# Kernel optimization log

Measured on AMD Instinct MI355X. Metric: run time of the kernel, lower is better.

The kernel has to match this reference:

```python
import jax, jax.numpy as jnp
import numpy as np

SHAPELET_SIZE = 64
NUM_SHAPELETS = 128
IN_CHANNELS = 8


def setup_inputs() -> dict:
    key = jax.random.key(0)
    k1, k2 = jax.random.split(key)
    x = jax.random.normal(k1, (64, IN_CHANNELS, 2048), dtype=jnp.float32)
    shapelets = jax.random.normal(k2, (IN_CHANNELS, NUM_SHAPELETS, SHAPELET_SIZE), dtype=jnp.float32)
    return {"x": x, "shapelets": shapelets}


def _znorm(s):
    # Z-normalize along the time-step axis (dim 2), matching Znormalize_dim(shapelets, 2)
    mu = jnp.mean(s, axis=2, keepdims=True)
    sd = jnp.std(s, axis=2, keepdims=True)
    return (s - mu) / sd


def reference(x, shapelets):
    # x: (N, C, L); shapelets: (C, K, S)
    S = shapelets.shape[-1]
    N, C, L = x.shape
    W = L - S + 1
    # unfold(2, S, 1): sliding windows -> (N, C, W, S)
    idx = jnp.arange(W)[:, None] + jnp.arange(S)[None, :]  # (W, S)
    xw = x[:, :, idx]  # (N, C, W, S)
    sh = _znorm(shapelets)  # (C, K, S)
    # Euclidean cdist via ||a||^2 + ||b||^2 - 2 a.b (avoids (N,C,W,K,S) blowup)
    sq_x = jnp.sum(xw * xw, axis=-1)          # (N, C, W)
    sq_s = jnp.sum(sh * sh, axis=-1)          # (C, K)
    cross = jnp.einsum('ncws,cks->ncwk', xw, sh)  # (N, C, W, K)
    d2 = sq_x[..., None] + sq_s[None, :, None, :] - 2.0 * cross
    d = jnp.sqrt(jnp.maximum(d2, 1e-12))      # (N, C, W, K)
    # sum over channels, then global min over windows -> (N, 1, K)
    dsum = jnp.sum(d, axis=1)                 # (N, W, K)
    out = jnp.min(dsum, axis=1)[:, None, :]   # (N, 1, K)
    return out
```

## Files before the change

kernel.cpp:

```cpp
#include <hip/hip_runtime.h>
#include <hip/hip_bf16.h>
#include <math.h>

#define C 8
#define K 128
#define S 64
#define L 2048
#define NB 64
#define W (L - S + 1)
#define TW 128
#define NTW 16
#define NKB 2
#define XCS 208
#define XFS 200

typedef __attribute__((ext_vector_type(8))) short bf16x8;
typedef __attribute__((ext_vector_type(4))) float f32x4;

__device__ __forceinline__ unsigned short f2bf(float f) {
  unsigned int u = __float_as_uint(f);
  u += 0x7FFFu + ((u >> 16) & 1u);
  return (unsigned short)(u >> 16);
}

__device__ __forceinline__ unsigned int pkbf(float a, float b) {
  __hip_bfloat162 h = __float22bfloat162_rn(make_float2(a, b));
  return *reinterpret_cast<unsigned int*>(&h);
}

__device__ __forceinline__ void gll16(const void* g, void* l) {
  __builtin_amdgcn_global_load_lds((const __attribute__((address_space(1))) void*)g,
                                   (__attribute__((address_space(3))) void*)l, 16, 0, 0);
}

__global__ __launch_bounds__(256) void prep_kernel(const float* __restrict__ sh,
                                                   unsigned short* __restrict__ shzB,
                                                   float* __restrict__ out) {
  int tid = blockIdx.x * 256 + threadIdx.x;
  if (tid < NB * K) out[tid] = __int_as_float(0x7F800000);
  int gid = blockIdx.x * 4 + (threadIdx.x >> 6);
  int lane = threadIdx.x & 63;
  float v = sh[(size_t)gid * S + lane];
  float s1 = v, s2 = v * v;
#pragma unroll
  for (int off = 32; off > 0; off >>= 1) {
    s1 += __shfl_down(s1, off);
    s2 += __shfl_down(s2, off);
  }
  s1 = __shfl(s1, 0);
  s2 = __shfl(s2, 0);
  float mu = s1 * (1.0f / S);
  float sd = sqrtf(fmaxf(s2 * (1.0f / S) - mu * mu, 0.0f));
  float z = (v - mu) / sd;
  int c = gid >> 7, k = gid & (K - 1), s = lane;
  int idx = (k >> 6) * 32768 + c * 4096 + ((((k >> 4) & 3) * 2) + (s >> 5)) * 512 +
            ((((s >> 3) & 3) * 16 + (k & 15)) * 8) + (s & 7);
  shzB[idx] = f2bf(-2.0f * z);
}

__global__ __launch_bounds__(512, 4) void main_kernel(const float* __restrict__ x,
                                                      const unsigned short* __restrict__ shzB,
                                                      int* __restrict__ out) {
  __shared__ __align__(16) unsigned short bbuf[4096];
  __shared__ __align__(16) unsigned short xcop[C][8][XCS];
  __shared__ __align__(16) float sqx[C][TW];

  const int t = threadIdx.x;
  const int lane = t & 63;
  const int wave = t >> 6;
  const int wgrp = wave & 1;
  const int kgrp = wave >> 1;
  const int col = lane & 15;
  const int quad = lane >> 4;
  const int n = blockIdx.z;
  const int kblk = blockIdx.y;
  const int w0 = blockIdx.x * TW;
  const float* xn = x + (size_t)n * C * L;
  const unsigned short* bsrc = shzB + kblk * 32768;

  float* xf = (float*)bbuf;
  {
    const int c = wave;
    const int e = lane * 4;
    float4 v; v.x = v.y = v.z = v.w = 0.0f;
    if (lane < 48) {
      int g = w0 + e;
      if (g + 3 < L) {
        v = *(const float4*)(xn + c * L + g);
      } else {
        v.x = (g + 0 < L) ? xn[c * L + g + 0] : 0.0f;
        v.y = (g + 1 < L) ? xn[c * L + g + 1] : 0.0f;
        v.z = (g + 2 < L) ? xn[c * L + g + 2] : 0.0f;
        v.w = (g + 3 < L) ? xn[c * L + g + 3] : 0.0f;
      }
    }
    if (lane < 50) *(float4*)&xf[c * XFS + e] = v;
  }
  __syncthreads();

  {
    const int cb = wave;
    const int rb = lane >> 3;
    const int c8 = lane & 7;
    const float* xr = xf + cb * XFS;
#pragma unroll
    for (int j = 0; j < 12; ++j) {
      int i = (c8 + j * 8) * 2;
      *(unsigned int*)&xcop[cb][rb][i] = pkbf(xr[i + rb], xr[i + rb + 1]);
    }
  }
  {
    const int c = wave, wl = lane * 2;
    const float* xr = xf + c * XFS;
    float p0 = 0.f, p1 = 0.f, p2 = 0.f, p3 = 0.f;
#pragma unroll
    for (int si = 0; si < S; si += 4) {
      float v0 = xr[wl + si], v1 = xr[wl + si + 1], v2 = xr[wl + si + 2], v3 = xr[wl + si + 3];
      p0 = fmaf(v0, v0, p0); p1 = fmaf(v1, v1, p1);
      p2 = fmaf(v2, v2, p2); p3 = fmaf(v3, v3, p3);
    }
    float s0 = 64.0f + (p0 + p1) + (p2 + p3);
    sqx[c][wl] = s0;
    float a = xr[wl + S], b = xr[wl];
    sqx[c][wl + 1] = s0 + a * a - b * b;
  }
  __syncthreads();

  gll16(bsrc + t * 8, &bbuf[wave * 512]);

  const f32x4 z4 = {0.0f, 0.0f, 0.0f, 0.0f};
  f32x4 dsum[4];
#pragma unroll
  for (int a = 0; a < 4; ++a) dsum[a] = z4;

  const int r8 = col & 7;
  const int abase = wgrp * 64 + (col - r8) + quad * 8;

  for (int c = 0; c < C; ++c) {
    __syncthreads();
    bf16x8 b0 = *(const bf16x8*)(&bbuf[(kgrp * 2 + 0) * 512 + lane * 8]);
    bf16x8 b1 = *(const bf16x8*)(&bbuf[(kgrp * 2 + 1) * 512 + lane * 8]);
    __syncthreads();

    if (c + 1 < C)
      gll16(bsrc + (c + 1) * 4096 + t * 8, &bbuf[wave * 512]);

    f32x4 acc[4];
#pragma unroll
    for (int wt = 0; wt < 4; ++wt)
      acc[wt] = *(const f32x4*)&sqx[c][wgrp * 64 + wt * 16 + quad * 4];
    const unsigned short* xc = &xcop[c][r8][0];
#pragma unroll
    for (int wt = 0; wt < 4; ++wt) {
      bf16x8 a0 = *(const bf16x8*)(xc + abase + wt * 16);
      acc[wt] = __builtin_amdgcn_mfma_f32_16x16x32_bf16(a0, b0, acc[wt], 0, 0, 0);
    }
#pragma unroll
    for (int wt = 0; wt < 4; ++wt) {
      bf16x8 a1 = *(const bf16x8*)(xc + abase + wt * 16 + 32);
      acc[wt] = __builtin_amdgcn_mfma_f32_16x16x32_bf16(a1, b1, acc[wt], 0, 0, 0);
    }
#pragma unroll
    for (int wt = 0; wt < 4; ++wt)
#pragma unroll
      for (int i = 0; i < 4; ++i)
        dsum[wt][i] += __builtin_amdgcn_sqrtf(fmaxf(acc[wt][i], 0.0f));
  }

  const float INF = __int_as_float(0x7F800000);
  int wbase = w0 + wgrp * 64;
  float mv = INF;
#pragma unroll
  for (int wt = 0; wt < 4; ++wt)
#pragma unroll
    for (int i = 0; i < 4; ++i) {
      int w = wbase + wt * 16 + quad * 4 + i;
      mv = (w < W) ? fminf(mv, dsum[wt][i]) : mv;
    }
  mv = fminf(mv, __shfl_xor(mv, 16));
  mv = fminf(mv, __shfl_xor(mv, 32));
  if (quad == 0)
    atomicMin(&out[n * K + kblk * 64 + kgrp * 16 + col], __float_as_int(mv));
}

extern "C" void kernel_launch(void* const* d_in, const int* in_sizes, int n_in,
                              void* d_out, int out_size, void* d_ws, size_t ws_size,
                              hipStream_t stream) {
  const float* x = (const float*)d_in[0];
  const float* sh = (const float*)d_in[1];
  float* out = (float*)d_out;
  unsigned short* shzB = (unsigned short*)d_ws;

  prep_kernel<<<256, 256, 0, stream>>>(sh, shzB, out);
  main_kernel<<<dim3(NTW, NKB, NB), 512, 0, stream>>>(x, shzB, (int*)out);
}
```

Baseline: 91.78 us.

## Cover all shapelets per block with 4 k-tiles per wave and double-buffered B

Removes the k-block grid dimension so each 256-thread block handles all 128 shapelets for one window tile. Each wave now computes four 16-wide k tiles, which reuses the A fragments from LDS across four MFMAs, and the per-channel shapelet tiles are double-buffered in LDS so one sync per channel is enough. This halves redundant x loading and packing across blocks, at the cost of more accumulator registers, lower occupancy, and half as many blocks.

```diff
diff --git a/kernel.cpp b/kernel.cpp
--- a/kernel.cpp
+++ b/kernel.cpp
@@ -10,7 +10,6 @@
 #define W (L - S + 1)
 #define TW 128
 #define NTW 16
-#define NKB 2
 #define XCS 208
 #define XFS 200
 
@@ -53,15 +52,15 @@
   float sd = sqrtf(fmaxf(s2 * (1.0f / S) - mu * mu, 0.0f));
   float z = (v - mu) / sd;
   int c = gid >> 7, k = gid & (K - 1), s = lane;
-  int idx = (k >> 6) * 32768 + c * 4096 + ((((k >> 4) & 3) * 2) + (s >> 5)) * 512 +
+  int idx = c * 8192 + (k >> 6) * 4096 + ((((k >> 4) & 3) * 2) + (s >> 5)) * 512 +
             ((((s >> 3) & 3) * 16 + (k & 15)) * 8) + (s & 7);
   shzB[idx] = f2bf(-2.0f * z);
 }
 
-__global__ __launch_bounds__(512, 4) void main_kernel(const float* __restrict__ x,
+__global__ __launch_bounds__(256, 2) void main_kernel(const float* __restrict__ x,
                                                       const unsigned short* __restrict__ shzB,
                                                       int* __restrict__ out) {
-  __shared__ __align__(16) unsigned short bbuf[4096];
+  __shared__ __align__(16) unsigned short bbuf[2][8192];
   __shared__ __align__(16) unsigned short xcop[C][8][XCS];
   __shared__ __align__(16) float sqx[C][TW];
 
@@ -72,15 +71,15 @@
   const int kgrp = wave >> 1;
   const int col = lane & 15;
   const int quad = lane >> 4;
-  const int n = blockIdx.z;
-  const int kblk = blockIdx.y;
+  const int n = blockIdx.y;
   const int w0 = blockIdx.x * TW;
   const float* xn = x + (size_t)n * C * L;
-  const unsigned short* bsrc = shzB + kblk * 32768;
+  const unsigned short* bsrc = shzB;
 
   float* xf = (float*)bbuf;
-  {
-    const int c = wave;
+#pragma unroll
+  for (int cc = 0; cc < 2; ++cc) {
+    const int c = wave * 2 + cc;
     const int e = lane * 4;
     float4 v; v.x = v.y = v.z = v.w = 0.0f;
     if (lane < 48) {
@@ -98,8 +97,9 @@
   }
   __syncthreads();
 
-  {
-    const int cb = wave;
+#pragma unroll
+  for (int cc = 0; cc < 2; ++cc) {
+    const int cb = wave * 2 + cc;
     const int rb = lane >> 3;
     const int c8 = lane & 7;
     const float* xr = xf + cb * XFS;
@@ -109,8 +109,9 @@
       *(unsigned int*)&xcop[cb][rb][i] = pkbf(xr[i + rb], xr[i + rb + 1]);
     }
   }
-  {
-    const int c = wave, wl = lane * 2;
+#pragma unroll
+  for (int cc = 0; cc < 2; ++cc) {
+    const int c = wave * 2 + cc, wl = lane * 2;
     const float* xr = xf + c * XFS;
     float p0 = 0.f, p1 = 0.f, p2 = 0.f, p3 = 0.f;
 #pragma unroll
@@ -126,61 +127,81 @@
   }
   __syncthreads();
 
-  gll16(bsrc + t * 8, &bbuf[wave * 512]);
+#pragma unroll
+  for (int i = 0; i < 4; ++i)
+    gll16(bsrc + i * 2048 + t * 8, &bbuf[0][i * 2048 + wave * 512]);
 
   const f32x4 z4 = {0.0f, 0.0f, 0.0f, 0.0f};
-  f32x4 dsum[4];
-#pragma unroll
-  for (int a = 0; a < 4; ++a) dsum[a] = z4;
+  f32x4 dsum[4][4];
+#pragma unroll
+  for (int kt = 0; kt < 4; ++kt)
+#pragma unroll
+    for (int wt = 0; wt < 4; ++wt) dsum[kt][wt] = z4;
 
   const int r8 = col & 7;
   const int abase = wgrp * 64 + (col - r8) + quad * 8;
 
   for (int c = 0; c < C; ++c) {
     __syncthreads();
-    bf16x8 b0 = *(const bf16x8*)(&bbuf[(kgrp * 2 + 0) * 512 + lane * 8]);
-    bf16x8 b1 = *(const bf16x8*)(&bbuf[(kgrp * 2 + 1) * 512 + lane * 8]);
-    __syncthreads();
-
-    if (c + 1 < C)
-      gll16(bsrc + (c + 1) * 4096 + t * 8, &bbuf[wave * 512]);
-
-    f32x4 acc[4];
+
+    if (c + 1 < C) {
+#pragma unroll
+      for (int i = 0; i < 4; ++i)
+        gll16(bsrc + (c + 1) * 8192 + i * 2048 + t * 8,
+              &bbuf[(c + 1) & 1][i * 2048 + wave * 512]);
+    }
+
+    const unsigned short* bb = &bbuf[c & 1][kgrp * 4096];
+    bf16x8 b00 = *(const bf16x8*)(bb + 0 * 512 + lane * 8);
+    bf16x8 b01 = *(const bf16x8*)(bb + 1 * 512 + lane * 8);
+    bf16x8 b10 = *(const bf16x8*)(bb + 2 * 512 + lane * 8);
+    bf16x8 b11 = *(const bf16x8*)(bb + 3 * 512 + lane * 8);
+    bf16x8 b20 = *(const bf16x8*)(bb + 4 * 512 + lane * 8);
+    bf16x8 b21 = *(const bf16x8*)(bb + 5 * 512 + lane * 8);
+    bf16x8 b30 = *(const bf16x8*)(bb + 6 * 512 + lane * 8);
+    bf16x8 b31 = *(const bf16x8*)(bb + 7 * 512 + lane * 8);
+
+    const unsigned short* xc = &xcop[c][r8][0];
+#pragma unroll
+    for (int wt = 0; wt < 4; ++wt) {
+      f32x4 ai = *(const f32x4*)&sqx[c][wgrp * 64 + wt * 16 + quad * 4];
+      bf16x8 x0 = *(const bf16x8*)(xc + abase + wt * 16);
+      bf16x8 x1 = *(const bf16x8*)(xc + abase + wt * 16 + 32);
+      f32x4 a0 = __builtin_amdgcn_mfma_f32_16x16x32_bf16(x0, b00, ai, 0, 0, 0);
+      f32x4 a1 = __builtin_amdgcn_mfma_f32_16x16x32_bf16(x0, b10, ai, 0, 0, 0);
+      f32x4 a2 = __builtin_amdgcn_mfma_f32_16x16x32_bf16(x0, b20, ai, 0, 0, 0);
+      f32x4 a3 = __builtin_amdgcn_mfma_f32_16x16x32_bf16(x0, b30, ai, 0, 0, 0);
+      a0 = __builtin_amdgcn_mfma_f32_16x16x32_bf16(x1, b01, a0, 0, 0, 0);
+      a1 = __builtin_amdgcn_mfma_f32_16x16x32_bf16(x1, b11, a1, 0, 0, 0);
+      a2 = __builtin_amdgcn_mfma_f32_16x16x32_bf16(x1, b21, a2, 0, 0, 0);
+      a3 = __builtin_amdgcn_mfma_f32_16x16x32_bf16(x1, b31, a3, 0, 0, 0);
+#pragma unroll
+      for (int i = 0; i < 4; ++i) {
+        dsum[0][wt][i] += __builtin_amdgcn_sqrtf(fmaxf(a0[i], 0.0f));
+        dsum[1][wt][i] += __builtin_amdgcn_sqrtf(fmaxf(a1[i], 0.0f));
+        dsum[2][wt][i] += __builtin_amdgcn_sqrtf(fmaxf(a2[i], 0.0f));
+        dsum[3][wt][i] += __builtin_amdgcn_sqrtf(fmaxf(a3[i], 0.0f));
+      }
+    }
+  }
+
+  const float INF = __int_as_float(0x7F800000);
+  const int wbase = w0 + wgrp * 64;
+#pragma unroll
+  for (int kt = 0; kt < 4; ++kt) {
+    float mv = INF;
 #pragma unroll
     for (int wt = 0; wt < 4; ++wt)
-      acc[wt] = *(const f32x4*)&sqx[c][wgrp * 64 + wt * 16 + quad * 4];
-    const unsigned short* xc = &xcop[c][r8][0];
-#pragma unroll
-    for (int wt = 0; wt < 4; ++wt) {
-      bf16x8 a0 = *(const bf16x8*)(xc + abase + wt * 16);
-      acc[wt] = __builtin_amdgcn_mfma_f32_16x16x32_bf16(a0, b0, acc[wt], 0, 0, 0);
-    }
-#pragma unroll
-    for (int wt = 0; wt < 4; ++wt) {
-      bf16x8 a1 = *(const bf16x8*)(xc + abase + wt * 16 + 32);
-      acc[wt] = __builtin_amdgcn_mfma_f32_16x16x32_bf16(a1, b1, acc[wt], 0, 0, 0);
-    }
-#pragma unroll
-    for (int wt = 0; wt < 4; ++wt)
-#pragma unroll
-      for (int i = 0; i < 4; ++i)
-        dsum[wt][i] += __builtin_amdgcn_sqrtf(fmaxf(acc[wt][i], 0.0f));
-  }
-
-  const float INF = __int_as_float(0x7F800000);
-  int wbase = w0 + wgrp * 64;
-  float mv = INF;
-#pragma unroll
-  for (int wt = 0; wt < 4; ++wt)
-#pragma unroll
-    for (int i = 0; i < 4; ++i) {
-      int w = wbase + wt * 16 + quad * 4 + i;
-      mv = (w < W) ? fminf(mv, dsum[wt][i]) : mv;
-    }
-  mv = fminf(mv, __shfl_xor(mv, 16));
-  mv = fminf(mv, __shfl_xor(mv, 32));
-  if (quad == 0)
-    atomicMin(&out[n * K + kblk * 64 + kgrp * 16 + col], __float_as_int(mv));
+#pragma unroll
+      for (int i = 0; i < 4; ++i) {
+        int w = wbase + wt * 16 + quad * 4 + i;
+        mv = (w < W) ? fminf(mv, dsum[kt][wt][i]) : mv;
+      }
+    mv = fminf(mv, __shfl_xor(mv, 16));
+    mv = fminf(mv, __shfl_xor(mv, 32));
+    if (quad == 0)
+      atomicMin(&out[n * K + kgrp * 64 + kt * 16 + col], __float_as_int(mv));
+  }
 }
 
 extern "C" void kernel_launch(void* const* d_in, const int* in_sizes, int n_in,
@@ -192,5 +213,5 @@
   unsigned short* shzB = (unsigned short*)d_ws;
 
   prep_kernel<<<256, 256, 0, stream>>>(sh, shzB, out);
-  main_kernel<<<dim3(NTW, NKB, NB), 512, 0, stream>>>(x, shzB, (int*)out);
-}
+  main_kernel<<<dim3(NTW, NB), 256, 0, stream>>>(x, shzB, (int*)out);
+}
```

Result: no change. 92.28 us (+0.6%).

## Split waves into MFMA producers and sqrt consumers via double-buffered LDS slab

Applied to the files above, without the earlier changes.

Each block now covers all 128 shapelets instead of half. Four waves compute the MFMA distances into a double-buffered LDS slab while the other four waves, at raised priority, apply sqrt and accumulate across channels. B fragments are loaded directly from global memory into registers instead of through LDS, and each block starts at a rotated channel so blocks spread their reads. This aims to overlap the transcendental work with the matrix work and halve the redundant x staging, but it raises LDS use and drops occupancy to one block of 512 threads per CU.

```diff
diff --git a/kernel.cpp b/kernel.cpp
--- a/kernel.cpp
+++ b/kernel.cpp
@@ -10,9 +10,9 @@
 #define W (L - S + 1)
 #define TW 128
 #define NTW 16
-#define NKB 2
 #define XCS 208
 #define XFS 200
+#define SW 72
 
 typedef __attribute__((ext_vector_type(8))) short bf16x8;
 typedef __attribute__((ext_vector_type(4))) float f32x4;
@@ -26,11 +26,6 @@
 __device__ __forceinline__ unsigned int pkbf(float a, float b) {
   __hip_bfloat162 h = __float22bfloat162_rn(make_float2(a, b));
   return *reinterpret_cast<unsigned int*>(&h);
-}
-
-__device__ __forceinline__ void gll16(const void* g, void* l) {
-  __builtin_amdgcn_global_load_lds((const __attribute__((address_space(1))) void*)g,
-                                   (__attribute__((address_space(3))) void*)l, 16, 0, 0);
 }
 
 __global__ __launch_bounds__(256) void prep_kernel(const float* __restrict__ sh,
@@ -53,32 +48,69 @@
   float sd = sqrtf(fmaxf(s2 * (1.0f / S) - mu * mu, 0.0f));
   float z = (v - mu) / sd;
   int c = gid >> 7, k = gid & (K - 1), s = lane;
-  int idx = (k >> 6) * 32768 + c * 4096 + ((((k >> 4) & 3) * 2) + (s >> 5)) * 512 +
+  int idx = c * 8192 + (k >> 6) * 4096 + ((((k >> 4) & 3) * 2) + (s >> 5)) * 512 +
             ((((s >> 3) & 3) * 16 + (k & 15)) * 8) + (s & 7);
   shzB[idx] = f2bf(-2.0f * z);
 }
 
-__global__ __launch_bounds__(512, 4) void main_kernel(const float* __restrict__ x,
+#define PRODUCE(H, SLOT)                                                        \
+  {                                                                             \
+    const unsigned short* xc = &xcop[c][r8][0];                                 \
+    const int wb = (H) * 64 + pw2 * 32;                                         \
+    _Pragma("unroll")                                                           \
+    for (int wt = 0; wt < 2; ++wt) {                                            \
+      f32x4 ai = *(const f32x4*)&sqx[c][wb + wt * 16 + quad * 4];               \
+      bf16x8 x0 = *(const bf16x8*)(xc + alane + wb + wt * 16);                  \
+      bf16x8 x1 = *(const bf16x8*)(xc + alane + wb + wt * 16 + 32);             \
+      _Pragma("unroll")                                                         \
+      for (int kt = 0; kt < 4; ++kt) {                                          \
+        f32x4 acc =                                                             \
+            __builtin_amdgcn_mfma_f32_16x16x32_bf16(x0, Bc[2 * kt], ai, 0, 0, 0);\
+        acc = __builtin_amdgcn_mfma_f32_16x16x32_bf16(x1, Bc[2 * kt + 1], acc,  \
+                                                      0, 0, 0);                 \
+        *(f32x4*)&slab[SLOT][pk * 64 + kt * 16 + col]                           \
+                           [pw2 * 32 + wt * 16 + quad * 4] = acc;               \
+      }                                                                         \
+    }                                                                           \
+  }
+
+#define CONSUME(SLOT, DS)                                                       \
+  {                                                                             \
+    f32x4 r[4][2];                                                              \
+    _Pragma("unroll")                                                           \
+    for (int wt = 0; wt < 4; ++wt)                                              \
+      _Pragma("unroll")                                                         \
+      for (int kl = 0; kl < 2; ++kl)                                            \
+        r[wt][kl] = *(const f32x4*)&slab[SLOT][q * 32 + kl * 16 + col]          \
+                                             [wt * 16 + quad * 4];              \
+    _Pragma("unroll")                                                           \
+    for (int wt = 0; wt < 4; ++wt)                                              \
+      _Pragma("unroll")                                                         \
+      for (int kl = 0; kl < 2; ++kl)                                            \
+        _Pragma("unroll")                                                       \
+        for (int i = 0; i < 4; ++i)                                             \
+          DS[wt][kl][i] +=                                                      \
+              __builtin_amdgcn_sqrtf(__builtin_fabsf(r[wt][kl][i]));            \
+  }
+
+__global__ __launch_bounds__(512, 1) void main_kernel(const float* __restrict__ x,
                                                       const unsigned short* __restrict__ shzB,
                                                       int* __restrict__ out) {
-  __shared__ __align__(16) unsigned short bbuf[4096];
+  __shared__ __align__(16) float slab[2][K][SW];
   __shared__ __align__(16) unsigned short xcop[C][8][XCS];
   __shared__ __align__(16) float sqx[C][TW];
 
   const int t = threadIdx.x;
   const int lane = t & 63;
   const int wave = t >> 6;
-  const int wgrp = wave & 1;
-  const int kgrp = wave >> 1;
   const int col = lane & 15;
   const int quad = lane >> 4;
-  const int n = blockIdx.z;
-  const int kblk = blockIdx.y;
+  const int n = blockIdx.y;
   const int w0 = blockIdx.x * TW;
   const float* xn = x + (size_t)n * C * L;
-  const unsigned short* bsrc = shzB + kblk * 32768;
-
-  float* xf = (float*)bbuf;
+  const int cbase = (blockIdx.x + 3 * blockIdx.y) & 7;
+
+  float* xfp = &slab[0][0][0];
   {
     const int c = wave;
     const int e = lane * 4;
@@ -94,7 +126,7 @@
         v.w = (g + 3 < L) ? xn[c * L + g + 3] : 0.0f;
       }
     }
-    if (lane < 50) *(float4*)&xf[c * XFS + e] = v;
+    if (lane < 50) *(float4*)&xfp[c * XFS + e] = v;
   }
   __syncthreads();
 
@@ -102,7 +134,7 @@
     const int cb = wave;
     const int rb = lane >> 3;
     const int c8 = lane & 7;
-    const float* xr = xf + cb * XFS;
+    const float* xr = xfp + cb * XFS;
 #pragma unroll
     for (int j = 0; j < 12; ++j) {
       int i = (c8 + j * 8) * 2;
@@ -111,7 +143,7 @@
   }
   {
     const int c = wave, wl = lane * 2;
-    const float* xr = xf + c * XFS;
+    const float* xr = xfp + c * XFS;
     float p0 = 0.f, p1 = 0.f, p2 = 0.f, p3 = 0.f;
 #pragma unroll
     for (int si = 0; si < S; si += 4) {
@@ -124,63 +156,71 @@
     float a = xr[wl + S], b = xr[wl];
     sqx[c][wl + 1] = s0 + a * a - b * b;
   }
+
+  const int r8 = col & 7;
+  const int alane = (col - r8) + quad * 8;
+
+  const int pk = wave >> 1;
+  const int pw2 = wave & 1;
+  const unsigned short* bwp = shzB + pk * 4096 + lane * 8;
+
+  const int q = wave & 3;
+  const f32x4 z4 = {0.0f, 0.0f, 0.0f, 0.0f};
+  f32x4 ds0[4][2], ds1[4][2];
+#pragma unroll
+  for (int wt = 0; wt < 4; ++wt)
+#pragma unroll
+    for (int kl = 0; kl < 2; ++kl) { ds0[wt][kl] = z4; ds1[wt][kl] = z4; }
+
+  if (wave >= 4) __builtin_amdgcn_s_setprio(1);
+
+  for (int ci = 0; ci < 8; ++ci) {
+    const int c = (cbase + ci) & 7;
+
+    bf16x8 Bc[8];
+    if (wave < 4) {
+#pragma unroll
+      for (int i = 0; i < 8; ++i)
+        Bc[i] = *(const bf16x8*)(bwp + c * 8192 + i * 512);
+    }
+
+    __syncthreads();
+    if (wave < 4) {
+      PRODUCE(0, 0)
+    } else if (ci > 0) {
+      CONSUME(1, ds1)
+    }
+
+    __syncthreads();
+    if (wave < 4) {
+      PRODUCE(1, 1)
+    } else {
+      CONSUME(0, ds0)
+    }
+  }
   __syncthreads();
-
-  gll16(bsrc + t * 8, &bbuf[wave * 512]);
-
-  const f32x4 z4 = {0.0f, 0.0f, 0.0f, 0.0f};
-  f32x4 dsum[4];
-#pragma unroll
-  for (int a = 0; a < 4; ++a) dsum[a] = z4;
-
-  const int r8 = col & 7;
-  const int abase = wgrp * 64 + (col - r8) + quad * 8;
-
-  for (int c = 0; c < C; ++c) {
-    __syncthreads();
-    bf16x8 b0 = *(const bf16x8*)(&bbuf[(kgrp * 2 + 0) * 512 + lane * 8]);
-    bf16x8 b1 = *(const bf16x8*)(&bbuf[(kgrp * 2 + 1) * 512 + lane * 8]);
-    __syncthreads();
-
-    if (c + 1 < C)
-      gll16(bsrc + (c + 1) * 4096 + t * 8, &bbuf[wave * 512]);
-
-    f32x4 acc[4];
-#pragma unroll
-    for (int wt = 0; wt < 4; ++wt)
-      acc[wt] = *(const f32x4*)&sqx[c][wgrp * 64 + wt * 16 + quad * 4];
-    const unsigned short* xc = &xcop[c][r8][0];
-#pragma unroll
-    for (int wt = 0; wt < 4; ++wt) {
-      bf16x8 a0 = *(const bf16x8*)(xc + abase + wt * 16);
-      acc[wt] = __builtin_amdgcn_mfma_f32_16x16x32_bf16(a0, b0, acc[wt], 0, 0, 0);
-    }
-#pragma unroll
-    for (int wt = 0; wt < 4; ++wt) {
-      bf16x8 a1 = *(const bf16x8*)(xc + abase + wt * 16 + 32);
-      acc[wt] = __builtin_amdgcn_mfma_f32_16x16x32_bf16(a1, b1, acc[wt], 0, 0, 0);
-    }
-#pragma unroll
-    for (int wt = 0; wt < 4; ++wt)
-#pragma unroll
-      for (int i = 0; i < 4; ++i)
-        dsum[wt][i] += __builtin_amdgcn_sqrtf(fmaxf(acc[wt][i], 0.0f));
-  }
-
-  const float INF = __int_as_float(0x7F800000);
-  int wbase = w0 + wgrp * 64;
-  float mv = INF;
-#pragma unroll
-  for (int wt = 0; wt < 4; ++wt)
-#pragma unroll
-    for (int i = 0; i < 4; ++i) {
-      int w = wbase + wt * 16 + quad * 4 + i;
-      mv = (w < W) ? fminf(mv, dsum[wt][i]) : mv;
-    }
-  mv = fminf(mv, __shfl_xor(mv, 16));
-  mv = fminf(mv, __shfl_xor(mv, 32));
-  if (quad == 0)
-    atomicMin(&out[n * K + kblk * 64 + kgrp * 16 + col], __float_as_int(mv));
+  if (wave >= 4) {
+    CONSUME(1, ds1)
+
+    const float INF = __int_as_float(0x7F800000);
+#pragma unroll
+    for (int kl = 0; kl < 2; ++kl) {
+      float mv = INF;
+#pragma unroll
+      for (int wt = 0; wt < 4; ++wt)
+#pragma unroll
+        for (int i = 0; i < 4; ++i) {
+          int wA = w0 + wt * 16 + quad * 4 + i;
+          int wB = wA + 64;
+          mv = (wA < W) ? fminf(mv, ds0[wt][kl][i]) : mv;
+          mv = (wB < W) ? fminf(mv, ds1[wt][kl][i]) : mv;
+        }
+      mv = fminf(mv, __shfl_xor(mv, 16));
+      mv = fminf(mv, __shfl_xor(mv, 32));
+      if (quad == 0)
+        atomicMin(&out[n * K + q * 32 + kl * 16 + col], __float_as_int(mv));
+    }
+  }
 }
 
 extern "C" void kernel_launch(void* const* d_in, const int* in_sizes, int n_in,
@@ -192,5 +232,5 @@
   unsigned short* shzB = (unsigned short*)d_ws;
 
   prep_kernel<<<256, 256, 0, stream>>>(sh, shzB, out);
-  main_kernel<<<dim3(NTW, NKB, NB), 512, 0, stream>>>(x, shzB, (int*)out);
-}
+  main_kernel<<<dim3(NTW, NB), 512, 0, stream>>>(x, shzB, (int*)out);
+}
```

Result: slower. 105.6 us (+15.1%).
